# Kernel tuning notes

Measured on AMD Instinct MI355X. Metric: run time of the kernel, lower is better.

## Reference

```python
import jax, jax.numpy as jnp
from jax import lax
import numpy as np

L = 6            # layer_number
CHEB2 = 4        # chebyshev_number ** 2
C = 4 * CHEB2    # per-block channel size = 16
G = 2 ** L       # final block grid = 64 (freq_len / leftover)


def _pool_avg2(y):
    # AvgPool2d kernel=2 stride=2 (dims always divisible here)
    B, Ch, H, W = y.shape
    return y.reshape(B, Ch, H // 2, 2, W // 2, 2).mean(axis=(3, 5))


def _wrap_pad1(y):
    # period_padding by 1 on bottom/right (circular)
    return jnp.pad(y, ((0, 0), (0, 0), (0, 1), (0, 1)), mode='wrap')


def _conv(x, w, groups=1):
    return lax.conv_general_dilated(x, w, (1, 1), 'VALID', feature_group_count=groups)


def _forward(x, W0, b0, Wr, br, Wft, bft):
    B = x.shape[0]
    z0 = jnp.zeros_like(x)
    # split: real input -> (Re+, Re-, Im+=0, Im-=0) per channel (in_channel=1)
    y = jnp.concatenate([jax.nn.relu(x), jax.nn.relu(-x), z0, z0], axis=1)  # [B,4,64,64]
    # layer 0: kernel (w_h,w_w)=(2,2), 4 -> 4*4*cheb^2 = 64
    y = _conv(y, W0) + b0[None, :, None, None]  # [B,64,63,63]
    y = jax.nn.relu(y)
    y = _pool_avg2(_wrap_pad1(y))               # [B,64,32,32] = 2^(L-1) grid
    # recursion layers: per-block 2x2 conv C -> 4C, batched as grouped conv
    for lyr in range(1, L):
        g = 2 ** lyr
        nb = g * g
        z = _conv(y, Wr[lyr - 1], groups=nb) + br[lyr - 1][None, :, None, None]
        s = z.shape[-1]                          # 2^(L-lyr) - 1
        # grouped-conv channel order [A_y, A_x, y_loc, x_loc, C] ->
        # target block index 2^(lyr+1)*(2*A_y+y_loc) + (2*A_x+x_loc):
        z = z.reshape(B, g, g, 2, 2, C, s, s).transpose(0, 1, 3, 2, 4, 5, 6, 7)
        z = z.reshape(B, nb * 4 * C, s, s)
        z = jax.nn.relu(z)
        y = _pool_avg2(_wrap_pad1(z))            # spatial halves -> 2^(L-lyr-1)
    # FT layer: 4^L blocks, 1x1 conv C -> 4*leftover^2 = 4, spatial is 1x1
    v = y.reshape(B, G * G, C)
    f = jnp.einsum('bnc,noc->bno', v, Wft) + bft[None]  # [B,4096,4]
    f = f.reshape(B, G, G, 4)                            # (ky, kx) frequency grid
    real = f[..., 0] - f[..., 1]
    imag = f[..., 2] - f[..., 3]
    return jnp.stack([real, imag], axis=1)               # [B,2,64,64]


def setup_inputs() -> dict:
    key = jax.random.key(0)
    ks = jax.random.split(key, 16)
    sc = 0.1
    inp = {
        'x':  jax.random.normal(ks[0], (256, 1, 64, 64), jnp.float32),
        'W0': sc * jax.random.normal(ks[1], (64, 4, 2, 2), jnp.float32),
        'b0': sc * jax.random.normal(ks[2], (64,), jnp.float32),
        'Wft': sc * jax.random.normal(ks[3], (4096, 4, 16), jnp.float32),
        'bft': sc * jax.random.normal(ks[4], (4096, 4), jnp.float32),
    }
    for lyr in range(1, L):
        nb = 4 ** lyr
        inp[f'W{lyr}'] = sc * jax.random.normal(ks[4 + 2 * lyr - 1], (nb * 4 * C, C, 2, 2), jnp.float32)
        inp[f'b{lyr}'] = sc * jax.random.normal(ks[4 + 2 * lyr], (nb * 4 * C,), jnp.float32)
    return inp


def reference(x, W0, b0, W1, b1, W2, b2, W3, b3, W4, b4, W5, b5, Wft, bft):
    Wr = (W1, W2, W3, W4, W5)
    br = (b1, b2, b3, b4, b5)
    return _forward(x, W0, b0, Wr, br, Wft, bft)
```

## Files before the change

### kernel.cpp

```cpp
#include <hip/hip_runtime.h>
#include <hip/hip_bf16.h>


typedef __attribute__((ext_vector_type(4))) float f32x4;
typedef __attribute__((ext_vector_type(8))) short s16x8;

__device__ __forceinline__ short f2bf(float f) {
  union { float f; unsigned u; } v; v.f = f;
  unsigned r = v.u + 0x7fff + ((v.u >> 16) & 1);
  return (short)(r >> 16);
}
__device__ __forceinline__ float bf2f(short s) {
  union { unsigned u; float f; } v; v.u = ((unsigned)(unsigned short)s) << 16;
  return v.f;
}
constexpr int ilog2c(int v) { return v <= 1 ? 0 : 1 + ilog2c(v / 2); }

#define WOFF1 0
#define WOFF2 16384
#define WOFF3 81920
#define WOFF4 344064
#define WOFF5 1392640
#define WTOT  5586944

__global__ __launch_bounds__(256) void k_wconv(
    const float* __restrict__ W1, const float* __restrict__ W2,
    const float* __restrict__ W3, const float* __restrict__ W4,
    const float* __restrict__ W5, short* __restrict__ wbf) {
  const int idx = blockIdx.x * 256 + threadIdx.x;
  if (idx >= WTOT) return;
  const float* src;
  int local;
  if (idx < WOFF2)      { src = W1; local = idx; }
  else if (idx < WOFF3) { src = W2; local = idx - WOFF2; }
  else if (idx < WOFF4) { src = W3; local = idx - WOFF3; }
  else if (idx < WOFF5) { src = W4; local = idx - WOFF4; }
  else                  { src = W5; local = idx - WOFF5; }
  const int gi = local >> 12, i = local & 4095;
  const int j = i & 7, row = (i >> 3) & 15, g = (i >> 7) & 3, dy = (i >> 9) & 1, t = i >> 10;
  const int k = 8 * g + j, ic = k & 15, dx = k >> 4;
  wbf[idx] = f2bf(src[(size_t)gi * 4096 + ((t * 16 + row) * 16 + ic) * 4 + dy * 2 + dx]);
}

__global__ __launch_bounds__(256) void k_layer0(
    const float* __restrict__ x, const float* __restrict__ W0,
    const float* __restrict__ b0, short* __restrict__ out) {
  constexpr int GS = 4112;
  __shared__ __align__(16) float xs[17 * 64];
  __shared__ __align__(16) short os[4 * GS];
  const int b = blockIdx.x, p0 = blockIdx.y * 8;
  const float* xb = x + (size_t)b * 4096;
  for (int i = threadIdx.x; i < 17 * 16; i += 256) {
    int lr = i >> 4, c4 = i & 15;
    ((float4*)xs)[i] = *(const float4*)(xb + ((2 * p0 + lr) & 63) * 64 + c4 * 4);
  }
  __syncthreads();
  const int oc = threadIdx.x & 63, wv = threadIdx.x >> 6;
  const int g = oc >> 4, c = oc & 15;
  float wp[2][2], wm[2][2];
#pragma unroll
  for (int kh = 0; kh < 2; ++kh)
#pragma unroll
    for (int kw = 0; kw < 2; ++kw) {
      wp[kh][kw] = W0[((oc * 4 + 0) * 2 + kh) * 2 + kw];
      wm[kh][kw] = W0[((oc * 4 + 1) * 2 + kh) * 2 + kw];
    }
  const float bias = b0[oc];
  for (int t = wv; t < 64; t += 4) {
    const int phl = t >> 3, c0 = (t & 7) * 8;
    const int lrA = 2 * phl;
    float vA[9], vB[9], vC[9];
#pragma unroll
    for (int j = 0; j < 8; ++j) {
      vA[j] = xs[lrA * 64 + c0 + j];
      vB[j] = xs[(lrA + 1) * 64 + c0 + j];
      vC[j] = xs[(lrA + 2) * 64 + c0 + j];
    }
    vA[8] = xs[lrA * 64 + ((c0 + 8) & 63)];
    vB[8] = xs[(lrA + 1) * 64 + ((c0 + 8) & 63)];
    vC[8] = xs[(lrA + 2) * 64 + ((c0 + 8) & 63)];
    float pA[9], mA[9], pB[9], mB[9], pC[9], mC[9];
#pragma unroll
    for (int j = 0; j < 9; ++j) {
      pA[j] = fmaxf(vA[j], 0.f); mA[j] = pA[j] - vA[j];
      pB[j] = fmaxf(vB[j], 0.f); mB[j] = pB[j] - vB[j];
      pC[j] = fmaxf(vC[j], 0.f); mC[j] = pC[j] - vC[j];
    }
    float sc0[8], sc1[8];
#pragma unroll
    for (int q = 0; q < 8; ++q) {
      sc0[q] = bias + wp[0][0] * pA[q] + wm[0][0] * mA[q] + wp[0][1] * pA[q + 1] + wm[0][1] * mA[q + 1]
                    + wp[1][0] * pB[q] + wm[1][0] * mB[q] + wp[1][1] * pB[q + 1] + wm[1][1] * mB[q + 1];
      sc1[q] = bias + wp[0][0] * pB[q] + wm[0][0] * mB[q] + wp[0][1] * pB[q + 1] + wm[0][1] * mB[q + 1]
                    + wp[1][0] * pC[q] + wm[1][0] * mC[q] + wp[1][1] * pC[q + 1] + wm[1][1] * mC[q + 1];
    }
#pragma unroll
    for (int p = 0; p < 4; ++p) {
      float po = 0.25f * (fmaxf(sc0[2 * p], 0.f) + fmaxf(sc0[2 * p + 1], 0.f) +
                          fmaxf(sc1[2 * p], 0.f) + fmaxf(sc1[2 * p + 1], 0.f));
      os[g * GS + (phl * 32 + c0 / 2 + p) * 16 + c] = f2bf(po);
    }
  }
  __syncthreads();
#pragma unroll
  for (int gg = 0; gg < 4; ++gg) {
    short* dst = out + ((size_t)b * 4 + gg) * 16384 + (size_t)p0 * 512;
    for (int i = threadIdx.x; i < 512; i += 256)
      *(float4*)&dst[i * 8] = *(const float4*)&os[gg * GS + i * 8];
  }
}

template <int S, int G, int ITW>
__global__ __launch_bounds__(256) void k_bconv(
    const short* __restrict__ yin, const short* __restrict__ wbf,
    const float* __restrict__ Bv, short* __restrict__ yout) {
  constexpr int NB = G * G;
  constexpr int SO = S / 2;
  constexpr int LOG_SO = ilog2c(SO);
  const int gi = blockIdx.y;
  const int lane = threadIdx.x & 63, wv = threadIdx.x >> 6;
  const int lp = lane & 15, g4 = lane >> 4;
  const int dxg = g4 >> 1, ich = g4 & 1;

  const short* wl = wbf + (size_t)gi * 4096;
  s16x8 af[4][2];
#pragma unroll
  for (int t = 0; t < 4; ++t)
#pragma unroll
    for (int dy = 0; dy < 2; ++dy)
      af[t][dy] = *(const s16x8*)&wl[(((t * 2 + dy) * 4 + g4) * 16 + lp) * 8];
  f32x4 bv[4];
#pragma unroll
  for (int t = 0; t < 4; ++t)
    bv[t] = *(const f32x4*)&Bv[(size_t)gi * 64 + t * 16 + g4 * 4];

  const int A_y = gi / G, A_x = gi - A_y * G;
  const int chunk0 = (blockIdx.x * 4 + wv) * ITW;

#pragma unroll
  for (int it = 0; it < ITW; ++it) {
    const int pg = (chunk0 + it) * 16 + lp;
    const int px = pg & (SO - 1);
    const int py = (pg >> LOG_SO) & (SO - 1);
    const int bi = pg >> (2 * LOG_SO);
    const size_t base = ((size_t)bi * NB + gi) * (S * S * 16) + ich * 8;
    s16x8 bf[3][2];
#pragma unroll
    for (int rr = 0; rr < 3; ++rr) {
      const int r = (2 * py + rr) & (S - 1);
#pragma unroll
      for (int cc = 0; cc < 2; ++cc) {
        const int c = (2 * px + dxg + cc) & (S - 1);
        bf[rr][cc] = *(const s16x8*)&yin[base + (size_t)(r * S + c) * 16];
      }
    }
    f32x4 acc[4][4];
#pragma unroll
    for (int t = 0; t < 4; ++t)
#pragma unroll
      for (int ph = 0; ph < 4; ++ph) acc[t][ph] = bv[t];
#pragma unroll
    for (int phy = 0; phy < 2; ++phy)
#pragma unroll
      for (int phx = 0; phx < 2; ++phx) {
        const int ph = phy * 2 + phx;
#pragma unroll
        for (int dy = 0; dy < 2; ++dy) {
          s16x8 frag = bf[phy + dy][phx];
#pragma unroll
          for (int t = 0; t < 4; ++t)
            acc[t][ph] = __builtin_amdgcn_mfma_f32_16x16x32_bf16(af[t][dy], frag, acc[t][ph], 0, 0, 0);
        }
      }
#pragma unroll
    for (int t = 0; t < 4; ++t) {
      short pk[4];
#pragma unroll
      for (int r = 0; r < 4; ++r) {
        float po = 0.25f * (fmaxf(acc[t][0][r], 0.f) + fmaxf(acc[t][1][r], 0.f) +
                            fmaxf(acc[t][2][r], 0.f) + fmaxf(acc[t][3][r], 0.f));
        pk[r] = f2bf(po);
      }
      const int gip = (A_y * 2 + (t >> 1)) * (2 * G) + A_x * 2 + (t & 1);
      size_t dst = (((size_t)bi * (4 * NB) + gip) * (SO * SO) + py * SO + px) * 16 + g4 * 4;
      *(short4*)&yout[dst] = make_short4(pk[0], pk[1], pk[2], pk[3]);
    }
  }
}

__global__ __launch_bounds__(256) void k_ft(
    const short* __restrict__ v, const float* __restrict__ Wft,
    const float* __restrict__ bft, float* __restrict__ out) {
  const int n = blockIdx.x * 64 + (threadIdx.x & 63);
  const int b0 = blockIdx.y * 32 + (threadIdx.x >> 6) * 8;
  float w[64];
  const float4* wp = (const float4*)(Wft + (size_t)n * 64);
#pragma unroll
  for (int j = 0; j < 16; ++j) {
    float4 t = wp[j];
    w[4 * j] = t.x; w[4 * j + 1] = t.y; w[4 * j + 2] = t.z; w[4 * j + 3] = t.w;
  }
  const float4 bq = *(const float4*)(bft + (size_t)n * 4);
#pragma unroll 2
  for (int bb = 0; bb < 8; ++bb) {
    const int b = b0 + bb;
    const short* vp = v + ((size_t)b * 4096 + n) * 16;
    s16x8 a0 = *(const s16x8*)vp;
    s16x8 a1 = *(const s16x8*)(vp + 8);
    float vv[16];
#pragma unroll
    for (int j = 0; j < 8; ++j) { vv[j] = bf2f(a0[j]); vv[8 + j] = bf2f(a1[j]); }
    float f0 = bq.x, f1 = bq.y, f2 = bq.z, f3 = bq.w;
#pragma unroll
    for (int j = 0; j < 16; ++j) {
      f0 += vv[j] * w[j];
      f1 += vv[j] * w[16 + j];
      f2 += vv[j] * w[32 + j];
      f3 += vv[j] * w[48 + j];
    }
    out[(size_t)b * 8192 + n] = f0 - f1;
    out[(size_t)b * 8192 + 4096 + n] = f2 - f3;
  }
}

extern "C" void kernel_launch(void* const* d_in, const int* in_sizes, int n_in,
                              void* d_out, int out_size, void* d_ws, size_t ws_size,
                              hipStream_t stream) {
  const float* x   = (const float*)d_in[0];
  const float* W0  = (const float*)d_in[1];
  const float* b0  = (const float*)d_in[2];
  const float* Wft = (const float*)d_in[3];
  const float* bft = (const float*)d_in[4];
  const float* W1 = (const float*)d_in[5];  const float* b1 = (const float*)d_in[6];
  const float* W2 = (const float*)d_in[7];  const float* b2 = (const float*)d_in[8];
  const float* W3 = (const float*)d_in[9];  const float* b3 = (const float*)d_in[10];
  const float* W4 = (const float*)d_in[11]; const float* b4 = (const float*)d_in[12];
  const float* W5 = (const float*)d_in[13]; const float* b5 = (const float*)d_in[14];

  short* buf0 = (short*)d_ws;
  short* buf1 = buf0 + (size_t)16777216;
  short* wbf  = buf1 + (size_t)16777216;

  k_wconv<<<(WTOT + 255) / 256, 256, 0, stream>>>(W1, W2, W3, W4, W5, wbf);
  k_layer0<<<dim3(256, 4), 256, 0, stream>>>(x, W0, b0, buf0);
  k_bconv<32, 2, 2><<<dim3(512, 4), 256, 0, stream>>>(buf0, wbf + WOFF1, b1, buf1);
  k_bconv<16, 4, 2><<<dim3(128, 16), 256, 0, stream>>>(buf1, wbf + WOFF2, b2, buf0);
  k_bconv<8, 8, 2><<<dim3(32, 64), 256, 0, stream>>>(buf0, wbf + WOFF3, b3, buf1);
  k_bconv<4, 16, 2><<<dim3(8, 256), 256, 0, stream>>>(buf1, wbf + WOFF4, b4, buf0);
  k_bconv<2, 32, 2><<<dim3(2, 1024), 256, 0, stream>>>(buf0, wbf + WOFF5, b5, buf1);
  k_ft<<<dim3(64, 8), 256, 0, stream>>>(buf1, Wft, bft, (float*)d_out);
}
```

Measured before the change: 233.4 us.

## Fuse weight conversion, recursion layers and FT into persistent kernel with grid barriers

```diff
diff --git a/kernel.cpp b/kernel.cpp
--- a/kernel.cpp
+++ b/kernel.cpp
@@ -22,29 +22,24 @@
 #define WOFF4 344064
 #define WOFF5 1392640
 #define WTOT  5586944
-
-__global__ __launch_bounds__(256) void k_wconv(
-    const float* __restrict__ W1, const float* __restrict__ W2,
-    const float* __restrict__ W3, const float* __restrict__ W4,
-    const float* __restrict__ W5, short* __restrict__ wbf) {
-  const int idx = blockIdx.x * 256 + threadIdx.x;
-  if (idx >= WTOT) return;
-  const float* src;
-  int local;
-  if (idx < WOFF2)      { src = W1; local = idx; }
-  else if (idx < WOFF3) { src = W2; local = idx - WOFF2; }
-  else if (idx < WOFF4) { src = W3; local = idx - WOFF3; }
-  else if (idx < WOFF5) { src = W4; local = idx - WOFF4; }
-  else                  { src = W5; local = idx - WOFF5; }
-  const int gi = local >> 12, i = local & 4095;
-  const int j = i & 7, row = (i >> 3) & 15, g = (i >> 7) & 3, dy = (i >> 9) & 1, t = i >> 10;
-  const int k = 8 * g + j, ic = k & 15, dx = k >> 4;
-  wbf[idx] = f2bf(src[(size_t)gi * 4096 + ((t * 16 + row) * 16 + ic) * 4 + dy * 2 + dx]);
+#define NBLK  256
+
+__device__ __forceinline__ void gridbar(unsigned* bar, unsigned target) {
+  __threadfence();
+  __syncthreads();
+  if (threadIdx.x == 0) {
+    atomicAdd(bar, 1u);
+    while (__hip_atomic_load(bar, __ATOMIC_RELAXED, __HIP_MEMORY_SCOPE_AGENT) < target)
+      __builtin_amdgcn_s_sleep(8);
+  }
+  __syncthreads();
+  __threadfence();
 }
 
 __global__ __launch_bounds__(256) void k_layer0(
     const float* __restrict__ x, const float* __restrict__ W0,
-    const float* __restrict__ b0, short* __restrict__ out) {
+    const float* __restrict__ b0, short* __restrict__ out, unsigned* __restrict__ bar) {
+  if (blockIdx.x == 0 && blockIdx.y == 0 && threadIdx.x == 0) *bar = 0u;
   constexpr int GS = 4112;
   __shared__ __align__(16) float xs[17 * 64];
   __shared__ __align__(16) short os[4 * GS];
@@ -110,19 +105,22 @@
   }
 }
 
-template <int S, int G, int ITW>
-__global__ __launch_bounds__(256) void k_bconv(
-    const short* __restrict__ yin, const short* __restrict__ wbf,
-    const float* __restrict__ Bv, short* __restrict__ yout) {
+template <int S, int G>
+__device__ __forceinline__ void layer_phase(
+    const short* __restrict__ yin, const short* __restrict__ wlayer,
+    const float* __restrict__ Bv, short* __restrict__ yout, int wave_global) {
   constexpr int NB = G * G;
   constexpr int SO = S / 2;
   constexpr int LOG_SO = ilog2c(SO);
-  const int gi = blockIdx.y;
-  const int lane = threadIdx.x & 63, wv = threadIdx.x >> 6;
+  constexpr int CPG = 16384 / NB;
+  const int lane = threadIdx.x & 63;
   const int lp = lane & 15, g4 = lane >> 4;
   const int dxg = g4 >> 1, ich = g4 & 1;
-
-  const short* wl = wbf + (size_t)gi * 4096;
+  const int chunk0 = wave_global * 16;
+  const int gi = chunk0 / CPG;
+  const int lc0 = chunk0 - gi * CPG;
+
+  const short* wl = wlayer + (size_t)gi * 4096;
   s16x8 af[4][2];
 #pragma unroll
   for (int t = 0; t < 4; ++t)
@@ -135,11 +133,10 @@
     bv[t] = *(const f32x4*)&Bv[(size_t)gi * 64 + t * 16 + g4 * 4];
 
   const int A_y = gi / G, A_x = gi - A_y * G;
-  const int chunk0 = (blockIdx.x * 4 + wv) * ITW;
-
-#pragma unroll
-  for (int it = 0; it < ITW; ++it) {
-    const int pg = (chunk0 + it) * 16 + lp;
+
+#pragma unroll 2
+  for (int it = 0; it < 16; ++it) {
+    const int pg = (lc0 + it) * 16 + lp;
     const int px = pg & (SO - 1);
     const int py = (pg >> LOG_SO) & (SO - 1);
     const int bi = pg >> (2 * LOG_SO);
@@ -188,38 +185,68 @@
   }
 }
 
-__global__ __launch_bounds__(256) void k_ft(
-    const short* __restrict__ v, const float* __restrict__ Wft,
-    const float* __restrict__ bft, float* __restrict__ out) {
-  const int n = blockIdx.x * 64 + (threadIdx.x & 63);
-  const int b0 = blockIdx.y * 32 + (threadIdx.x >> 6) * 8;
-  float w[64];
-  const float4* wp = (const float4*)(Wft + (size_t)n * 64);
-#pragma unroll
-  for (int j = 0; j < 16; ++j) {
-    float4 t = wp[j];
-    w[4 * j] = t.x; w[4 * j + 1] = t.y; w[4 * j + 2] = t.z; w[4 * j + 3] = t.w;
-  }
-  const float4 bq = *(const float4*)(bft + (size_t)n * 4);
+__global__ __launch_bounds__(256, 2) void k_mega(
+    const float* __restrict__ W1, const float* __restrict__ b1,
+    const float* __restrict__ W2, const float* __restrict__ b2,
+    const float* __restrict__ W3, const float* __restrict__ b3,
+    const float* __restrict__ W4, const float* __restrict__ b4,
+    const float* __restrict__ W5, const float* __restrict__ b5,
+    const float* __restrict__ Wft, const float* __restrict__ bft,
+    short* __restrict__ buf0, short* __restrict__ buf1,
+    short* __restrict__ wbf, float* __restrict__ out, unsigned* __restrict__ bar) {
+  for (int idx = blockIdx.x * 256 + threadIdx.x; idx < WTOT; idx += NBLK * 256) {
+    const float* src;
+    int local;
+    if (idx < WOFF2)      { src = W1; local = idx; }
+    else if (idx < WOFF3) { src = W2; local = idx - WOFF2; }
+    else if (idx < WOFF4) { src = W3; local = idx - WOFF3; }
+    else if (idx < WOFF5) { src = W4; local = idx - WOFF4; }
+    else                  { src = W5; local = idx - WOFF5; }
+    const int gi = local >> 12, i = local & 4095;
+    const int j = i & 7, row = (i >> 3) & 15, g = (i >> 7) & 3, dy = (i >> 9) & 1, t = i >> 10;
+    const int k = 8 * g + j, ic = k & 15, dx = k >> 4;
+    wbf[idx] = f2bf(src[(size_t)gi * 4096 + ((t * 16 + row) * 16 + ic) * 4 + dy * 2 + dx]);
+  }
+  gridbar(bar, NBLK * 1);
+
+  const int wave_global = blockIdx.x * 4 + (threadIdx.x >> 6);
+  layer_phase<32, 2>(buf0, wbf + WOFF1, b1, buf1, wave_global);  gridbar(bar, NBLK * 2);
+  layer_phase<16, 4>(buf1, wbf + WOFF2, b2, buf0, wave_global);  gridbar(bar, NBLK * 3);
+  layer_phase<8, 8>(buf0, wbf + WOFF3, b3, buf1, wave_global);   gridbar(bar, NBLK * 4);
+  layer_phase<4, 16>(buf1, wbf + WOFF4, b4, buf0, wave_global);  gridbar(bar, NBLK * 5);
+  layer_phase<2, 32>(buf0, wbf + WOFF5, b5, buf1, wave_global);  gridbar(bar, NBLK * 6);
+
+  {
+    const int n = (blockIdx.x & 63) * 64 + (threadIdx.x & 63);
+    const int b0i = (blockIdx.x >> 6) * 64 + (threadIdx.x >> 6) * 16;
+    float w[64];
+    const float4* wp = (const float4*)(Wft + (size_t)n * 64);
+#pragma unroll
+    for (int j = 0; j < 16; ++j) {
+      float4 t = wp[j];
+      w[4 * j] = t.x; w[4 * j + 1] = t.y; w[4 * j + 2] = t.z; w[4 * j + 3] = t.w;
+    }
+    const float4 bq = *(const float4*)(bft + (size_t)n * 4);
 #pragma unroll 2
-  for (int bb = 0; bb < 8; ++bb) {
-    const int b = b0 + bb;
-    const short* vp = v + ((size_t)b * 4096 + n) * 16;
-    s16x8 a0 = *(const s16x8*)vp;
-    s16x8 a1 = *(const s16x8*)(vp + 8);
-    float vv[16];
-#pragma unroll
-    for (int j = 0; j < 8; ++j) { vv[j] = bf2f(a0[j]); vv[8 + j] = bf2f(a1[j]); }
-    float f0 = bq.x, f1 = bq.y, f2 = bq.z, f3 = bq.w;
-#pragma unroll
-    for (int j = 0; j < 16; ++j) {
-      f0 += vv[j] * w[j];
-      f1 += vv[j] * w[16 + j];
-      f2 += vv[j] * w[32 + j];
-      f3 += vv[j] * w[48 + j];
-    }
-    out[(size_t)b * 8192 + n] = f0 - f1;
-    out[(size_t)b * 8192 + 4096 + n] = f2 - f3;
+    for (int bb = 0; bb < 16; ++bb) {
+      const int b = b0i + bb;
+      const short* vp = buf1 + ((size_t)b * 4096 + n) * 16;
+      s16x8 a0 = *(const s16x8*)vp;
+      s16x8 a1 = *(const s16x8*)(vp + 8);
+      float vv[16];
+#pragma unroll
+      for (int j = 0; j < 8; ++j) { vv[j] = bf2f(a0[j]); vv[8 + j] = bf2f(a1[j]); }
+      float f0 = bq.x, f1 = bq.y, f2 = bq.z, f3 = bq.w;
+#pragma unroll
+      for (int j = 0; j < 16; ++j) {
+        f0 += vv[j] * w[j];
+        f1 += vv[j] * w[16 + j];
+        f2 += vv[j] * w[32 + j];
+        f3 += vv[j] * w[48 + j];
+      }
+      out[(size_t)b * 8192 + n] = f0 - f1;
+      out[(size_t)b * 8192 + 4096 + n] = f2 - f3;
+    }
   }
 }
 
@@ -240,13 +267,9 @@
   short* buf0 = (short*)d_ws;
   short* buf1 = buf0 + (size_t)16777216;
   short* wbf  = buf1 + (size_t)16777216;
-
-  k_wconv<<<(WTOT + 255) / 256, 256, 0, stream>>>(W1, W2, W3, W4, W5, wbf);
-  k_layer0<<<dim3(256, 4), 256, 0, stream>>>(x, W0, b0, buf0);
-  k_bconv<32, 2, 2><<<dim3(512, 4), 256, 0, stream>>>(buf0, wbf + WOFF1, b1, buf1);
-  k_bconv<16, 4, 2><<<dim3(128, 16), 256, 0, stream>>>(buf1, wbf + WOFF2, b2, buf0);
-  k_bconv<8, 8, 2><<<dim3(32, 64), 256, 0, stream>>>(buf0, wbf + WOFF3, b3, buf1);
-  k_bconv<4, 16, 2><<<dim3(8, 256), 256, 0, stream>>>(buf1, wbf + WOFF4, b4, buf0);
-  k_bconv<2, 32, 2><<<dim3(2, 1024), 256, 0, stream>>>(buf0, wbf + WOFF5, b5, buf1);
-  k_ft<<<dim3(64, 8), 256, 0, stream>>>(buf1, Wft, bft, (float*)d_out);
-}
+  unsigned* bar = (unsigned*)(wbf + (size_t)((WTOT + 255) & ~255));
+
+  k_layer0<<<dim3(256, 4), 256, 0, stream>>>(x, W0, b0, buf0, bar);
+  k_mega<<<dim3(NBLK), 256, 0, stream>>>(W1, b1, W2, b2, W3, b3, W4, b4, W5, b5,
+                                         Wft, bft, buf0, buf1, wbf, (float*)d_out, bar);
+}
```

Result: slower. 551.3 us (+136.2%).

## Coalesce weight repack via LDS and flatten bconv grid with swizzled block mapping

Applied to the files above, without the earlier changes.

```diff
diff --git a/kernel.cpp b/kernel.cpp
--- a/kernel.cpp
+++ b/kernel.cpp
@@ -27,19 +27,37 @@
     const float* __restrict__ W1, const float* __restrict__ W2,
     const float* __restrict__ W3, const float* __restrict__ W4,
     const float* __restrict__ W5, short* __restrict__ wbf) {
-  const int idx = blockIdx.x * 256 + threadIdx.x;
-  if (idx >= WTOT) return;
-  const float* src;
-  int local;
-  if (idx < WOFF2)      { src = W1; local = idx; }
-  else if (idx < WOFF3) { src = W2; local = idx - WOFF2; }
-  else if (idx < WOFF4) { src = W3; local = idx - WOFF3; }
-  else if (idx < WOFF5) { src = W4; local = idx - WOFF4; }
-  else                  { src = W5; local = idx - WOFF5; }
-  const int gi = local >> 12, i = local & 4095;
-  const int j = i & 7, row = (i >> 3) & 15, g = (i >> 7) & 3, dy = (i >> 9) & 1, t = i >> 10;
-  const int k = 8 * g + j, ic = k & 15, dx = k >> 4;
-  wbf[idx] = f2bf(src[(size_t)gi * 4096 + ((t * 16 + row) * 16 + ic) * 4 + dy * 2 + dx]);
+  __shared__ short ws[4][4096];
+  const int tid = threadIdx.x;
+#pragma unroll
+  for (int lg = 0; lg < 4; ++lg) {
+    const int gg = blockIdx.x * 4 + lg;
+    const float* src;
+    int base;
+    if (gg < 4)        { src = W1; base = 0; }
+    else if (gg < 20)  { src = W2; base = 4; }
+    else if (gg < 84)  { src = W3; base = 20; }
+    else if (gg < 340) { src = W4; base = 84; }
+    else               { src = W5; base = 340; }
+    const float* gp = src + (size_t)(gg - base) * 4096;
+#pragma unroll
+    for (int q = 0; q < 4; ++q) {
+      float4 v = *(const float4*)(gp + tid * 16 + q * 4);
+      float vv[4] = {v.x, v.y, v.z, v.w};
+#pragma unroll
+      for (int e = 0; e < 4; ++e) {
+        const int s = tid * 16 + q * 4 + e;
+        const int oc = s >> 6, ic = (s >> 2) & 15, dy = (s >> 1) & 1, dx = s & 1;
+        const int t = oc >> 4, row = oc & 15;
+        const int k = dx * 16 + ic, g = k >> 3, j = k & 7;
+        ws[lg][(((t * 2 + dy) * 4 + g) * 16 + row) * 8 + j] = f2bf(vv[e]);
+      }
+    }
+  }
+  __syncthreads();
+  short* dst = wbf + (size_t)blockIdx.x * 16384;
+  for (int i = tid; i < 2048; i += 256)
+    ((float4*)dst)[i] = ((const float4*)&ws[0][0])[i];
 }
 
 __global__ __launch_bounds__(256) void k_layer0(
@@ -110,17 +128,22 @@
   }
 }
 
-template <int S, int G, int ITW>
+template <int S, int G>
 __global__ __launch_bounds__(256) void k_bconv(
     const short* __restrict__ yin, const short* __restrict__ wbf,
     const float* __restrict__ Bv, short* __restrict__ yout) {
   constexpr int NB = G * G;
   constexpr int SO = S / 2;
   constexpr int LOG_SO = ilog2c(SO);
-  const int gi = blockIdx.y;
+  constexpr int CPG = 16384 / NB;
+  constexpr int ITW = 4;
+  const int swz = (blockIdx.x & 7) * 128 + (blockIdx.x >> 3);
   const int lane = threadIdx.x & 63, wv = threadIdx.x >> 6;
   const int lp = lane & 15, g4 = lane >> 4;
   const int dxg = g4 >> 1, ich = g4 & 1;
+  const int chunk0 = (swz * 4 + wv) * ITW;
+  const int gi = chunk0 / CPG;
+  const int lc0 = chunk0 - gi * CPG;
 
   const short* wl = wbf + (size_t)gi * 4096;
   s16x8 af[4][2];
@@ -135,11 +158,10 @@
     bv[t] = *(const f32x4*)&Bv[(size_t)gi * 64 + t * 16 + g4 * 4];
 
   const int A_y = gi / G, A_x = gi - A_y * G;
-  const int chunk0 = (blockIdx.x * 4 + wv) * ITW;
-
-#pragma unroll
+
+#pragma unroll 2
   for (int it = 0; it < ITW; ++it) {
-    const int pg = (chunk0 + it) * 16 + lp;
+    const int pg = (lc0 + it) * 16 + lp;
     const int px = pg & (SO - 1);
     const int py = (pg >> LOG_SO) & (SO - 1);
     const int bi = pg >> (2 * LOG_SO);
@@ -241,12 +263,12 @@
   short* buf1 = buf0 + (size_t)16777216;
   short* wbf  = buf1 + (size_t)16777216;
 
-  k_wconv<<<(WTOT + 255) / 256, 256, 0, stream>>>(W1, W2, W3, W4, W5, wbf);
+  k_wconv<<<341, 256, 0, stream>>>(W1, W2, W3, W4, W5, wbf);
   k_layer0<<<dim3(256, 4), 256, 0, stream>>>(x, W0, b0, buf0);
-  k_bconv<32, 2, 2><<<dim3(512, 4), 256, 0, stream>>>(buf0, wbf + WOFF1, b1, buf1);
-  k_bconv<16, 4, 2><<<dim3(128, 16), 256, 0, stream>>>(buf1, wbf + WOFF2, b2, buf0);
-  k_bconv<8, 8, 2><<<dim3(32, 64), 256, 0, stream>>>(buf0, wbf + WOFF3, b3, buf1);
-  k_bconv<4, 16, 2><<<dim3(8, 256), 256, 0, stream>>>(buf1, wbf + WOFF4, b4, buf0);
-  k_bconv<2, 32, 2><<<dim3(2, 1024), 256, 0, stream>>>(buf0, wbf + WOFF5, b5, buf1);
+  k_bconv<32, 2><<<1024, 256, 0, stream>>>(buf0, wbf + WOFF1, b1, buf1);
+  k_bconv<16, 4><<<1024, 256, 0, stream>>>(buf1, wbf + WOFF2, b2, buf0);
+  k_bconv<8, 8><<<1024, 256, 0, stream>>>(buf0, wbf + WOFF3, b3, buf1);
+  k_bconv<4, 16><<<1024, 256, 0, stream>>>(buf1, wbf + WOFF4, b4, buf0);
+  k_bconv<2, 32><<<1024, 256, 0, stream>>>(buf0, wbf + WOFF5, b5, buf1);
   k_ft<<<dim3(64, 8), 256, 0, stream>>>(buf1, Wft, bft, (float*)d_out);
 }
```

After: 250.5 us. +7.3%, slower.
